# Kernel optimization log

Hardware: AMD Instinct MI355X
Metric: run time of the kernel (lower is better)

The kernel has to match this reference:

```python
import jax, jax.numpy as jnp
import numpy as np

B, N, H, A = 2048, 49, 1024, 512


def setup_inputs() -> dict:
    key = jax.random.key(0)
    ks = jax.random.split(key, 9)
    s_h = 1.0 / np.sqrt(H)
    s_a = 1.0 / np.sqrt(A)
    return {
        "hidden": jax.random.normal(ks[0], (B, H), jnp.float32),
        "img_features": jax.random.normal(ks[1], (B, N, H), jnp.float32),
        "coverage": jax.random.uniform(ks[2], (B, N), jnp.float32),
        "W_h": jax.random.uniform(ks[3], (H, A), jnp.float32, -s_h, s_h),
        "b_h": jax.random.uniform(ks[4], (A,), jnp.float32, -s_h, s_h),
        "W_img": jax.random.uniform(ks[5], (H, A), jnp.float32, -s_h, s_h),
        "b_img": jax.random.uniform(ks[6], (A,), jnp.float32, -s_h, s_h),
        "W_cov": jax.random.uniform(ks[7], (1, A), jnp.float32, -1.0, 1.0),
        "v": jax.random.uniform(ks[8], (A,), jnp.float32, -s_a, s_a),
    }


def reference(hidden, img_features, coverage, W_h, b_h, W_img, b_img, W_cov, v):
    # h_proj: (B, 1, A); img_proj: (B, N, A)
    h_proj = (hidden @ W_h + b_h)[:, None, :]
    img_proj = jnp.einsum("bnh,ha->bna", img_features, W_img) + b_img
    # coverage projection: (B, N, 1) @ (1, A) -> (B, N, A)
    cov_proj = coverage[:, :, None] * W_cov[0]
    energy = jnp.tanh(h_proj + img_proj + cov_proj)
    scores = jnp.einsum("bna,a->bn", energy, v)  # (B, N)
    alpha = jax.nn.softmax(scores, axis=1)
    context = jnp.einsum("bn,bnh->bh", alpha, img_features)
    return (context, alpha)
```

## Files before the change

### kernel.cpp

```cpp
#include <hip/hip_runtime.h>
#include <cstdint>
#include <cstddef>

#define B_ 2048
#define N_ 49
#define H_ 1024
#define A_ 512
#define M_ (B_*N_)

typedef __attribute__((ext_vector_type(8))) short short8;
typedef __attribute__((ext_vector_type(8))) unsigned short ushort8;
typedef __attribute__((ext_vector_type(4))) float f32x4;
typedef unsigned int u32;

__device__ inline unsigned short f2bf(float f){
  union { float f; unsigned u; } v; v.f = f;
  unsigned r = v.u + 0x7FFFu + ((v.u >> 16) & 1u);
  return (unsigned short)(r >> 16);
}
__device__ inline float bf2f(unsigned short h){
  union { u32 u; float f; } v; v.u = ((u32)h) << 16; return v.f;
}
__device__ inline float fast_tanh(float x){
  float e = __expf(2.0f*x);
  return 1.0f - 2.0f/(e + 1.0f);
}
__device__ inline void gl16(const void* g, void* l){
  __builtin_amdgcn_global_load_lds((const __attribute__((address_space(1))) u32*)g,
                                   (__attribute__((address_space(3))) u32*)l, 16, 0, 0);
}

__global__ __launch_bounds__(256) void k_transpose(
    const float* __restrict__ Wh, const float* __restrict__ Wimg,
    unsigned short* __restrict__ WtH, unsigned short* __restrict__ WtImg){
  const float* src = blockIdx.y ? Wimg : Wh;
  unsigned short* dst = blockIdx.y ? WtImg : WtH;
  int tk = (blockIdx.x & 31) * 32;
  int ta = (blockIdx.x >> 5) * 32;
  __shared__ unsigned short tile[32][33];
  int t = threadIdx.x;
  int r = t >> 3, c4 = t & 7;
  float4 vv = *(const float4*)(src + (size_t)(tk + r)*A_ + ta + c4*4);
  tile[c4*4+0][r] = f2bf(vv.x);
  tile[c4*4+1][r] = f2bf(vv.y);
  tile[c4*4+2][r] = f2bf(vv.z);
  tile[c4*4+3][r] = f2bf(vv.w);
  __syncthreads();
  ushort4 o;
  o.x = tile[r][c4*4+0]; o.y = tile[r][c4*4+1];
  o.z = tile[r][c4*4+2]; o.w = tile[r][c4*4+3];
  *(ushort4*)(dst + (size_t)(ta + r)*H_ + tk + c4*4) = o;
}

__global__ __launch_bounds__(256) void k_convert(
    const float* __restrict__ src, unsigned short* __restrict__ dst, size_t n8){
  size_t i = (size_t)blockIdx.x*256 + threadIdx.x;
  size_t stride = (size_t)gridDim.x*256;
  const float4* s4 = (const float4*)src;
  ushort8* d8 = (ushort8*)dst;
  for (; i < n8; i += stride){
    float4 a = s4[2*i], b = s4[2*i+1];
    ushort8 o;
    o[0]=f2bf(a.x); o[1]=f2bf(a.y); o[2]=f2bf(a.z); o[3]=f2bf(a.w);
    o[4]=f2bf(b.x); o[5]=f2bf(b.y); o[6]=f2bf(b.z); o[7]=f2bf(b.w);
    d8[i] = o;
  }
}

#define BK 64
#define LDK 72

__device__ inline void gemm_tile(const float* __restrict__ Asrc,
                                 const unsigned short* __restrict__ Wt,
                                 int m0, int a0, f32x4 acc[4][4],
                                 unsigned short (*sA)[LDK], unsigned short (*sB)[LDK]){
  const int t = threadIdx.x;
  const int l = t & 63, w = t >> 6;
  const int wr = w >> 1, wc = w & 1;
  const int g = l >> 4, c = l & 15;
  #pragma unroll
  for (int m=0;m<4;m++)
    #pragma unroll
    for (int n=0;n<4;n++)
      acc[m][n] = f32x4{0.f,0.f,0.f,0.f};

  for (int k0 = 0; k0 < H_; k0 += BK){
    #pragma unroll
    for (int i=0;i<8;i++){
      int f = i*256 + t;
      int row = f >> 4, c4 = f & 15;
      float4 vv = *(const float4*)(Asrc + (size_t)(m0+row)*H_ + k0 + c4*4);
      ushort4 h; h.x=f2bf(vv.x); h.y=f2bf(vv.y); h.z=f2bf(vv.z); h.w=f2bf(vv.w);
      *(ushort4*)&sA[row][c4*4] = h;
    }
    #pragma unroll
    for (int i=0;i<8;i++){
      int f = i*256 + t;
      int row = f >> 4, c4 = f & 15;
      *(ushort4*)&sB[row][c4*4] = *(const ushort4*)(Wt + (size_t)(a0+row)*H_ + k0 + c4*4);
    }
    __syncthreads();
    #pragma unroll
    for (int kk=0; kk<BK; kk+=32){
      short8 aF[4], bF[4];
      #pragma unroll
      for (int m=0;m<4;m++) aF[m] = *(const short8*)&sA[wr*64 + m*16 + c][kk + g*8];
      #pragma unroll
      for (int n=0;n<4;n++) bF[n] = *(const short8*)&sB[wc*64 + n*16 + c][kk + g*8];
      #pragma unroll
      for (int m=0;m<4;m++)
        #pragma unroll
        for (int n=0;n<4;n++)
          acc[m][n] = __builtin_amdgcn_mfma_f32_16x16x32_bf16(aF[m], bF[n], acc[m][n], 0, 0, 0);
    }
    __syncthreads();
  }
}

__global__ __launch_bounds__(256) void k_hproj(
    const float* __restrict__ hidden, const unsigned short* __restrict__ WtH,
    const float* __restrict__ b_h, float* __restrict__ hproj){
  __shared__ __align__(16) unsigned short sA[128][LDK];
  __shared__ __align__(16) unsigned short sB[128][LDK];
  f32x4 acc[4][4];
  int m0 = blockIdx.x * 128, a0 = blockIdx.y * 128;
  gemm_tile(hidden, WtH, m0, a0, acc, sA, sB);
  const int l = threadIdx.x & 63, w = threadIdx.x >> 6;
  const int wr = w >> 1, wc = w & 1, g = l >> 4, c = l & 15;
  #pragma unroll
  for (int n=0;n<4;n++){
    int col = a0 + wc*64 + n*16 + c;
    float bh = b_h[col];
    #pragma unroll
    for (int m=0;m<4;m++)
      #pragma unroll
      for (int r=0;r<4;r++){
        int rowg = m0 + wr*64 + m*16 + g*4 + r;
        hproj[(size_t)rowg*A_ + col] = acc[m][n][r] + bh;
      }
  }
}

__global__ __launch_bounds__(512, 2) void k_scores_p8(
    const unsigned short* __restrict__ Ab, const unsigned short* __restrict__ Wt,
    const float* __restrict__ hproj, const float* __restrict__ b_img,
    const float* __restrict__ cov, const float* __restrict__ Wcov,
    const float* __restrict__ v, float* __restrict__ scoresP){
  __shared__ __align__(16) char lds[131072];
  const int t = threadIdx.x;
  const int l = t & 63, w = t >> 6;
  const int wr = w >> 2, wc = w & 3;
  const int g = l >> 4, c = l & 15;
  const int cm = (c & 7) << 4;

  const int nwg = (M_/256)*(A_/256);
  int bid = blockIdx.x;
  int wg = (bid & 7)*(nwg/8) + (bid >> 3);
  const int m0 = (wg >> 1) * 256;
  const int a0 = (wg & 1) * 256;

  const int rsub = l >> 3;
  const int ksw  = ((l & 7) ^ rsub) * 8;

  f32x4 acc[8][4] = {};

  auto unit = [&](int d, int opoff, int h, int row0,
                  const unsigned short* src, int prow, int k0){
    gl16(src + (size_t)(prow + h*128 + row0 + w*8 + rsub)*H_ + k0 + ksw,
         lds + d*65536 + opoff + h*16384 + row0*128 + w*1024);
  };

  const int abase_s = wr*16384;
  const int bbase_s = 32768 + (wc>>1)*16384;
  const int brow    = (wc & 1)*64;

  auto phase_mfma = [&](int cur, int mh, int kb){
    short8 aF[4], bF[4];
    #pragma unroll
    for (int i=0;i<4;i++)
      aF[i] = *(const short8*)(lds + cur + abase_s + (mh*64 + i*16 + c)*128 + ((kb*64 + g*16) ^ cm));
    #pragma unroll
    for (int n=0;n<4;n++)
      bF[n] = *(const short8*)(lds + cur + bbase_s + (brow + n*16 + c)*128 + ((kb*64 + g*16) ^ cm));
    asm volatile("s_waitcnt lgkmcnt(0)" ::: "memory");
    __builtin_amdgcn_sched_barrier(0);
    __builtin_amdgcn_s_setprio(1);
    #pragma unroll
    for (int i=0;i<4;i++)
      #pragma unroll
      for (int n=0;n<4;n++)
        acc[mh*4+i][n] = __builtin_amdgcn_mfma_f32_16x16x32_bf16(aF[i], bF[n], acc[mh*4+i][n], 0, 0, 0);
    __builtin_amdgcn_s_setprio(0);
  };

  unit(0, 32768, 0, 0,  Wt, a0, 0);
  unit(0, 32768, 0, 64, Wt, a0, 0);
  unit(0, 32768, 1, 0,  Wt, a0, 0);
  unit(0, 32768, 1, 64, Wt, a0, 0);
  unit(0, 0,     0, 0,  Ab, m0, 0);
  unit(0, 0,     1, 0,  Ab, m0, 0);
  unit(0, 0,     0, 64, Ab, m0, 0);
  unit(0, 0,     1, 64, Ab, m0, 0);

  for (int tt=0; tt<16; ++tt){
    const int cur = (tt & 1) << 16;
    const int nd  = (tt + 1) & 1;
    const int nk  = (tt + 1) * 64;
    const bool pf = (tt < 15);

    if (pf){ unit(nd, 32768, 0, 0, Wt, a0, nk); unit(nd, 32768, 0, 64, Wt, a0, nk);
             asm volatile("s_waitcnt vmcnt(4)" ::: "memory"); }
    else   { asm volatile("s_waitcnt vmcnt(2)" ::: "memory"); }
    asm volatile("s_barrier" ::: "memory");
    phase_mfma(cur, 0, 0);
    asm volatile("s_barrier" ::: "memory");

    if (pf){ unit(nd, 32768, 1, 0, Wt, a0, nk); unit(nd, 32768, 1, 64, Wt, a0, nk); }
    asm volatile("s_barrier" ::: "memory");
    phase_mfma(cur, 0, 1);
    asm volatile("s_barrier" ::: "memory");

    if (pf){ unit(nd, 0, 0, 0, Ab, m0, nk); unit(nd, 0, 1, 0, Ab, m0, nk);
             asm volatile("s_waitcnt vmcnt(6)" ::: "memory"); }
    else   { asm volatile("s_waitcnt vmcnt(0)" ::: "memory"); }
    asm volatile("s_barrier" ::: "memory");
    phase_mfma(cur, 1, 0);
    asm volatile("s_barrier" ::: "memory");

    if (pf){ unit(nd, 0, 0, 64, Ab, m0, nk); unit(nd, 0, 1, 64, Ab, m0, nk); }
    asm volatile("s_barrier" ::: "memory");
    phase_mfma(cur, 1, 1);
    asm volatile("s_barrier" ::: "memory");
  }

  float* sS = (float*)lds;
  float* sH = (float*)lds + 256;
  const int bFirst = m0 / N_;
  const int nB = (m0 + 255)/N_ - bFirst + 1;
  if (t < 256) sS[t] = 0.f;
  for (int idx = t; idx < nB*256; idx += 512){
    int bb = idx >> 8, a = idx & 255;
    sH[bb*256 + a] = hproj[(size_t)(bFirst + bb)*A_ + a0 + a];
  }
  __syncthreads();

  float vv[4], bi[4], wcv[4];
  #pragma unroll
  for (int n=0;n<4;n++){
    int colg = a0 + wc*64 + n*16 + c;
    vv[n] = v[colg]; bi[n] = b_img[colg]; wcv[n] = Wcov[colg];
  }
  #pragma unroll
  for (int m=0;m<8;m++){
    #pragma unroll
    for (int r=0;r<4;r++){
      int rowl = wr*128 + m*16 + g*4 + r;
      int bb = (m0 + rowl) / N_ - bFirst;
      float cv = cov[m0 + rowl];
      float s = 0.f;
      #pragma unroll
      for (int n=0;n<4;n++){
        float x = acc[m][n][r] + sH[bb*256 + wc*64 + n*16 + c] + bi[n] + cv*wcv[n];
        s += fast_tanh(x) * vv[n];
      }
      s += __shfl_xor(s, 1, 16);
      s += __shfl_xor(s, 2, 16);
      s += __shfl_xor(s, 4, 16);
      s += __shfl_xor(s, 8, 16);
      if (c == 0) atomicAdd(&sS[rowl], s);
    }
  }
  __syncthreads();
  if (t < 256) scoresP[(size_t)(a0 >> 8)*M_ + m0 + t] = sS[t];
}

__global__ __launch_bounds__(256) void k_ctx_b(
    const unsigned short* __restrict__ imgb, const float* __restrict__ scoresP,
    float* __restrict__ outCtx, float* __restrict__ outAlpha){
  int b = blockIdx.x;
  __shared__ float sAl[N_];
  int t = threadIdx.x;
  if (t < 64){
    float s = -1e30f;
    if (t < N_){
      size_t rg = (size_t)b*N_ + t;
      s = scoresP[rg] + scoresP[(size_t)M_ + rg];
    }
    float m = s;
    #pragma unroll
    for (int off=32; off>=1; off>>=1) m = fmaxf(m, __shfl_xor(m, off));
    float e = (t < N_) ? __expf(s - m) : 0.f;
    float sum = e;
    #pragma unroll
    for (int off=32; off>=1; off>>=1) sum += __shfl_xor(sum, off);
    float al = e / sum;
    if (t < N_){ sAl[t] = al; outAlpha[(size_t)b*N_ + t] = al; }
  }
  __syncthreads();
  float4 acc = {0.f,0.f,0.f,0.f};
  #pragma unroll 7
  for (int n=0;n<N_;n++){
    float al = sAl[n];
    ushort4 x = *(const ushort4*)(imgb + ((size_t)b*N_ + n)*H_ + t*4);
    acc.x += al*bf2f(x.x); acc.y += al*bf2f(x.y);
    acc.z += al*bf2f(x.z); acc.w += al*bf2f(x.w);
  }
  *(float4*)(outCtx + (size_t)b*H_ + t*4) = acc;
}

__global__ __launch_bounds__(256) void k_scores_f(
    const float* __restrict__ img, const unsigned short* __restrict__ WtImg,
    const float* __restrict__ hproj, const float* __restrict__ b_img,
    const float* __restrict__ cov, const float* __restrict__ Wcov,
    const float* __restrict__ v, float* __restrict__ scores){
  __shared__ __align__(16) unsigned short sA[128][LDK];
  __shared__ __align__(16) unsigned short sB[128][LDK];
  __shared__ float sH[4][128];
  f32x4 acc[4][4];
  int m0 = blockIdx.x * 128, a0 = blockIdx.y * 128;
  gemm_tile(img, WtImg, m0, a0, acc, sA, sB);
  int bFirst = m0 / N_;
  int bLast  = (m0 + 127) / N_;
  int nB = bLast - bFirst + 1;
  for (int idx = threadIdx.x; idx < nB*128; idx += 256){
    int bb = idx >> 7, a = idx & 127;
    sH[bb][a] = hproj[(size_t)(bFirst + bb)*A_ + a0 + a];
  }
  __syncthreads();
  const int l = threadIdx.x & 63, w = threadIdx.x >> 6;
  const int wr = w >> 1, wc = w & 1, g = l >> 4, c = l & 15;
  float vv[4], bi[4], wcv[4];
  #pragma unroll
  for (int n=0;n<4;n++){
    int col = a0 + wc*64 + n*16 + c;
    vv[n] = v[col]; bi[n] = b_img[col]; wcv[n] = Wcov[col];
  }
  #pragma unroll
  for (int m=0;m<4;m++)
    #pragma unroll
    for (int r=0;r<4;r++){
      int rowg = m0 + wr*64 + m*16 + g*4 + r;
      int bb = rowg / N_;
      float cv = cov[rowg];
      float s = 0.f;
      #pragma unroll
      for (int n=0;n<4;n++){
        float x = acc[m][n][r] + sH[bb - bFirst][wc*64 + n*16 + c] + bi[n] + cv*wcv[n];
        s += fast_tanh(x) * vv[n];
      }
      s += __shfl_xor(s, 1, 16);
      s += __shfl_xor(s, 2, 16);
      s += __shfl_xor(s, 4, 16);
      s += __shfl_xor(s, 8, 16);
      if (c == 0) atomicAdd(&scores[rowg], s);
    }
}

__global__ __launch_bounds__(256) void k_ctx_f(
    const float* __restrict__ img, const float* __restrict__ scores,
    float* __restrict__ outCtx, float* __restrict__ outAlpha){
  int b = blockIdx.x;
  __shared__ float sAl[N_];
  int t = threadIdx.x;
  if (t < 64){
    float s = (t < N_) ? scores[(size_t)b*N_ + t] : -1e30f;
    float m = s;
    #pragma unroll
    for (int off=32; off>=1; off>>=1) m = fmaxf(m, __shfl_xor(m, off));
    float e = (t < N_) ? __expf(s - m) : 0.f;
    float sum = e;
    #pragma unroll
    for (int off=32; off>=1; off>>=1) sum += __shfl_xor(sum, off);
    float al = e / sum;
    if (t < N_){ sAl[t] = al; outAlpha[(size_t)b*N_ + t] = al; }
  }
  __syncthreads();
  const float4* ib = (const float4*)(img + (size_t)b*N_*H_);
  float4 acc = {0.f,0.f,0.f,0.f};
  for (int n=0;n<N_;n++){
    float al = sAl[n];
    float4 x = ib[n*(H_/4) + t];
    acc.x += al*x.x; acc.y += al*x.y; acc.z += al*x.z; acc.w += al*x.w;
  }
  *(float4*)(outCtx + (size_t)b*H_ + t*4) = acc;
}

extern "C" void kernel_launch(void* const* d_in, const int* in_sizes, int n_in,
                              void* d_out, int out_size, void* d_ws, size_t ws_size,
                              hipStream_t stream){
  const float* hidden = (const float*)d_in[0];
  const float* img    = (const float*)d_in[1];
  const float* cov    = (const float*)d_in[2];
  const float* W_h    = (const float*)d_in[3];
  const float* b_h    = (const float*)d_in[4];
  const float* W_img  = (const float*)d_in[5];
  const float* b_img  = (const float*)d_in[6];
  const float* W_cov  = (const float*)d_in[7];
  const float* v      = (const float*)d_in[8];

  char* ws = (char*)d_ws;
  unsigned short* WtH   = (unsigned short*)ws;
  unsigned short* WtImg = (unsigned short*)(ws + (1u<<20));
  float* hproj   = (float*)(ws + (2u<<20));
  float* scoresP = (float*)(ws + (6u<<20));
  unsigned short* imgb = (unsigned short*)(ws + (8u<<20));

  float* outCtx   = (float*)d_out;
  float* outAlpha = outCtx + (size_t)B_*H_;

  const size_t needed = (8ull<<20) + (size_t)M_*H_*2;

  k_transpose<<<dim3(512, 2), 256, 0, stream>>>(W_h, W_img, WtH, WtImg);
  k_hproj<<<dim3(B_/128, A_/128), 256, 0, stream>>>(hidden, WtH, b_h, hproj);

  if (ws_size >= needed){
    k_convert<<<2048, 256, 0, stream>>>(img, imgb, (size_t)M_*H_/8);
    k_scores_p8<<<(M_/256)*(A_/256), 512, 0, stream>>>(imgb, WtImg, hproj, b_img, cov, W_cov, v, scoresP);
    k_ctx_b<<<B_, 256, 0, stream>>>(imgb, scoresP, outCtx, outAlpha);
  } else {
    hipMemsetAsync(scoresP, 0, (size_t)M_*sizeof(float), stream);
    k_scores_f<<<dim3(M_/128, A_/128), 256, 0, stream>>>(img, WtImg, hproj, b_img, cov, W_cov, v, scoresP);
    k_ctx_f<<<B_, 256, 0, stream>>>(img, scoresP, outCtx, outAlpha);
  }
}
```

Baseline: 347.2 us.

## Fuse score GEMM, softmax and context into one per-batch-group kernel

Replaces the split scores kernel and the separate context kernel with a single kernel. Each block owns 5 whole batches (245 rows padded to 256) and loops over both A halves itself, reducing scores in LDS. It then does the softmax and the alpha-weighted context sum in the same block. This removes the partial-scores round trip through global memory and a second launch, and the context pass can reread image rows that were just loaded and are likely still cached. The next half's tile loads are issued before the first epilogue so they overlap it. In exchange about 4% of GEMM rows are padding, and the grid shrinks to 410 large blocks, which may balance poorly across CUs.

```diff
diff --git a/kernel.cpp b/kernel.cpp
--- a/kernel.cpp
+++ b/kernel.cpp
@@ -7,6 +7,8 @@
 #define H_ 1024
 #define A_ 512
 #define M_ (B_*N_)
+#define NBB 5
+#define NBLK ((B_ + NBB - 1)/NBB)
 
 typedef __attribute__((ext_vector_type(8))) short short8;
 typedef __attribute__((ext_vector_type(8))) unsigned short ushort8;
@@ -141,33 +143,45 @@
   }
 }
 
-__global__ __launch_bounds__(512, 2) void k_scores_p8(
-    const unsigned short* __restrict__ Ab, const unsigned short* __restrict__ Wt,
+__global__ __launch_bounds__(512, 2) void k_fused2(
+    const unsigned short* __restrict__ imgb, const unsigned short* __restrict__ Wt,
     const float* __restrict__ hproj, const float* __restrict__ b_img,
     const float* __restrict__ cov, const float* __restrict__ Wcov,
-    const float* __restrict__ v, float* __restrict__ scoresP){
+    const float* __restrict__ v,
+    float* __restrict__ outCtx, float* __restrict__ outAlpha){
   __shared__ __align__(16) char lds[131072];
+  __shared__ float sSx[256];
+  __shared__ float sHx[NBB][256];
+  __shared__ float sAl[256];
+
   const int t = threadIdx.x;
   const int l = t & 63, w = t >> 6;
   const int wr = w >> 2, wc = w & 3;
   const int g = l >> 4, c = l & 15;
   const int cm = (c & 7) << 4;
 
-  const int nwg = (M_/256)*(A_/256);
-  int bid = blockIdx.x;
-  int wg = (bid & 7)*(nwg/8) + (bid >> 3);
-  const int m0 = (wg >> 1) * 256;
-  const int a0 = (wg & 1) * 256;
+  const int bm = blockIdx.x;
+  const int bb0 = bm * NBB;
+  const int NB = min(NBB, B_ - bb0);
+  const int mrows = NB * N_;
+  const int m0 = bb0 * N_;
+
+  if (t < 256) sSx[t] = 0.f;
 
   const int rsub = l >> 3;
   const int ksw  = ((l & 7) ^ rsub) * 8;
 
-  f32x4 acc[8][4] = {};
-
-  auto unit = [&](int d, int opoff, int h, int row0,
-                  const unsigned short* src, int prow, int k0){
-    gl16(src + (size_t)(prow + h*128 + row0 + w*8 + rsub)*H_ + k0 + ksw,
-         lds + d*65536 + opoff + h*16384 + row0*128 + w*1024);
+  f32x4 acc[8][4];
+
+  auto unitB = [&](int d, int a0, int h, int row0, int k0){
+    gl16(Wt + (size_t)(a0 + h*128 + row0 + w*8 + rsub)*H_ + k0 + ksw,
+         lds + d*65536 + 32768 + h*16384 + row0*128 + w*1024);
+  };
+  auto unitA = [&](int d, int h, int row0, int k0){
+    int prow = m0 + h*128 + row0 + w*8 + rsub;
+    if (prow >= M_) prow = 0;
+    gl16(imgb + (size_t)prow*H_ + k0 + ksw,
+         lds + d*65536 + h*16384 + row0*128 + w*1024);
   };
 
   const int abase_s = wr*16384;
@@ -193,119 +207,131 @@
     __builtin_amdgcn_s_setprio(0);
   };
 
-  unit(0, 32768, 0, 0,  Wt, a0, 0);
-  unit(0, 32768, 0, 64, Wt, a0, 0);
-  unit(0, 32768, 1, 0,  Wt, a0, 0);
-  unit(0, 32768, 1, 64, Wt, a0, 0);
-  unit(0, 0,     0, 0,  Ab, m0, 0);
-  unit(0, 0,     1, 0,  Ab, m0, 0);
-  unit(0, 0,     0, 64, Ab, m0, 0);
-  unit(0, 0,     1, 64, Ab, m0, 0);
-
-  for (int tt=0; tt<16; ++tt){
-    const int cur = (tt & 1) << 16;
-    const int nd  = (tt + 1) & 1;
-    const int nk  = (tt + 1) * 64;
-    const bool pf = (tt < 15);
-
-    if (pf){ unit(nd, 32768, 0, 0, Wt, a0, nk); unit(nd, 32768, 0, 64, Wt, a0, nk);
-             asm volatile("s_waitcnt vmcnt(4)" ::: "memory"); }
-    else   { asm volatile("s_waitcnt vmcnt(2)" ::: "memory"); }
-    asm volatile("s_barrier" ::: "memory");
-    phase_mfma(cur, 0, 0);
-    asm volatile("s_barrier" ::: "memory");
-
-    if (pf){ unit(nd, 32768, 1, 0, Wt, a0, nk); unit(nd, 32768, 1, 64, Wt, a0, nk); }
-    asm volatile("s_barrier" ::: "memory");
-    phase_mfma(cur, 0, 1);
-    asm volatile("s_barrier" ::: "memory");
-
-    if (pf){ unit(nd, 0, 0, 0, Ab, m0, nk); unit(nd, 0, 1, 0, Ab, m0, nk);
-             asm volatile("s_waitcnt vmcnt(6)" ::: "memory"); }
-    else   { asm volatile("s_waitcnt vmcnt(0)" ::: "memory"); }
-    asm volatile("s_barrier" ::: "memory");
-    phase_mfma(cur, 1, 0);
-    asm volatile("s_barrier" ::: "memory");
-
-    if (pf){ unit(nd, 0, 0, 64, Ab, m0, nk); unit(nd, 0, 1, 64, Ab, m0, nk); }
-    asm volatile("s_barrier" ::: "memory");
-    phase_mfma(cur, 1, 1);
-    asm volatile("s_barrier" ::: "memory");
-  }
-
-  float* sS = (float*)lds;
-  float* sH = (float*)lds + 256;
-  const int bFirst = m0 / N_;
-  const int nB = (m0 + 255)/N_ - bFirst + 1;
-  if (t < 256) sS[t] = 0.f;
-  for (int idx = t; idx < nB*256; idx += 512){
-    int bb = idx >> 8, a = idx & 255;
-    sH[bb*256 + a] = hproj[(size_t)(bFirst + bb)*A_ + a0 + a];
-  }
-  __syncthreads();
-
-  float vv[4], bi[4], wcv[4];
-  #pragma unroll
-  for (int n=0;n<4;n++){
-    int colg = a0 + wc*64 + n*16 + c;
-    vv[n] = v[colg]; bi[n] = b_img[colg]; wcv[n] = Wcov[colg];
-  }
-  #pragma unroll
-  for (int m=0;m<8;m++){
-    #pragma unroll
-    for (int r=0;r<4;r++){
-      int rowl = wr*128 + m*16 + g*4 + r;
-      int bb = (m0 + rowl) / N_ - bFirst;
-      float cv = cov[m0 + rowl];
-      float s = 0.f;
-      #pragma unroll
-      for (int n=0;n<4;n++){
-        float x = acc[m][n][r] + sH[bb*256 + wc*64 + n*16 + c] + bi[n] + cv*wcv[n];
-        s += fast_tanh(x) * vv[n];
+  auto prologue = [&](int a0){
+    unitB(0, a0, 0, 0, 0);  unitB(0, a0, 0, 64, 0);
+    unitB(0, a0, 1, 0, 0);  unitB(0, a0, 1, 64, 0);
+    unitA(0, 0, 0, 0);      unitA(0, 1, 0, 0);
+    unitA(0, 0, 64, 0);     unitA(0, 1, 64, 0);
+  };
+
+  auto kloop = [&](int a0){
+    for (int tt=0; tt<16; ++tt){
+      const int cur = (tt & 1) << 16;
+      const int nd  = (tt + 1) & 1;
+      const int nk  = (tt + 1) * 64;
+      const bool pf = (tt < 15);
+
+      if (pf){ unitB(nd, a0, 0, 0, nk); unitB(nd, a0, 0, 64, nk);
+               asm volatile("s_waitcnt vmcnt(4)" ::: "memory"); }
+      else   { asm volatile("s_waitcnt vmcnt(2)" ::: "memory"); }
+      asm volatile("s_barrier" ::: "memory");
+      phase_mfma(cur, 0, 0);
+      asm volatile("s_barrier" ::: "memory");
+
+      if (pf){ unitB(nd, a0, 1, 0, nk); unitB(nd, a0, 1, 64, nk); }
+      asm volatile("s_barrier" ::: "memory");
+      phase_mfma(cur, 0, 1);
+      asm volatile("s_barrier" ::: "memory");
+
+      if (pf){ unitA(nd, 0, 0, nk); unitA(nd, 1, 0, nk);
+               asm volatile("s_waitcnt vmcnt(6)" ::: "memory"); }
+      else   { asm volatile("s_waitcnt vmcnt(0)" ::: "memory"); }
+      asm volatile("s_barrier" ::: "memory");
+      phase_mfma(cur, 1, 0);
+      asm volatile("s_barrier" ::: "memory");
+
+      if (pf){ unitA(nd, 0, 64, nk); unitA(nd, 1, 64, nk); }
+      asm volatile("s_barrier" ::: "memory");
+      phase_mfma(cur, 1, 1);
+      asm volatile("s_barrier" ::: "memory");
+    }
+  };
+
+  auto epi = [&](int a0){
+    for (int idx = t; idx < NB*256; idx += 512){
+      int bb = idx >> 8, a = idx & 255;
+      sHx[bb][a] = hproj[(size_t)(bb0 + bb)*A_ + a0 + a];
+    }
+    __syncthreads();
+    float vv[4], bi[4], wcv[4];
+    #pragma unroll
+    for (int n=0;n<4;n++){
+      int colg = a0 + wc*64 + n*16 + c;
+      vv[n] = v[colg]; bi[n] = b_img[colg]; wcv[n] = Wcov[colg];
+    }
+    #pragma unroll
+    for (int m=0;m<8;m++){
+      #pragma unroll
+      for (int r=0;r<4;r++){
+        int rowl = wr*128 + m*16 + g*4 + r;
+        if (rowl < mrows){
+          int bb = rowl / N_;
+          float cv = cov[m0 + rowl];
+          float s = 0.f;
+          #pragma unroll
+          for (int n=0;n<4;n++){
+            float x = acc[m][n][r] + sHx[bb][wc*64 + n*16 + c] + bi[n] + cv*wcv[n];
+            s += fast_tanh(x) * vv[n];
+          }
+          s += __shfl_xor(s, 1, 16);
+          s += __shfl_xor(s, 2, 16);
+          s += __shfl_xor(s, 4, 16);
+          s += __shfl_xor(s, 8, 16);
+          if (c == 0) atomicAdd(&sSx[rowl], s);
+        }
       }
-      s += __shfl_xor(s, 1, 16);
-      s += __shfl_xor(s, 2, 16);
-      s += __shfl_xor(s, 4, 16);
-      s += __shfl_xor(s, 8, 16);
-      if (c == 0) atomicAdd(&sS[rowl], s);
-    }
-  }
-  __syncthreads();
-  if (t < 256) scoresP[(size_t)(a0 >> 8)*M_ + m0 + t] = sS[t];
-}
-
-__global__ __launch_bounds__(256) void k_ctx_b(
-    const unsigned short* __restrict__ imgb, const float* __restrict__ scoresP,
-    float* __restrict__ outCtx, float* __restrict__ outAlpha){
-  int b = blockIdx.x;
-  __shared__ float sAl[N_];
-  int t = threadIdx.x;
-  if (t < 64){
-    float s = -1e30f;
-    if (t < N_){
-      size_t rg = (size_t)b*N_ + t;
-      s = scoresP[rg] + scoresP[(size_t)M_ + rg];
-    }
-    float m = s;
-    #pragma unroll
-    for (int off=32; off>=1; off>>=1) m = fmaxf(m, __shfl_xor(m, off));
-    float e = (t < N_) ? __expf(s - m) : 0.f;
+    }
+    __syncthreads();
+  };
+
+  #pragma unroll
+  for (int m=0;m<8;m++)
+    #pragma unroll
+    for (int n=0;n<4;n++) acc[m][n] = f32x4{0.f,0.f,0.f,0.f};
+  prologue(0);
+  kloop(0);
+  prologue(256);
+  epi(0);
+
+  #pragma unroll
+  for (int m=0;m<8;m++)
+    #pragma unroll
+    for (int n=0;n<4;n++) acc[m][n] = f32x4{0.f,0.f,0.f,0.f};
+  kloop(256);
+  epi(256);
+
+  if (w < NB){
+    int b = w;
+    float s = (l < N_) ? sSx[b*N_ + l] : -1e30f;
+    float mx = s;
+    #pragma unroll
+    for (int off=32; off>=1; off>>=1) mx = fmaxf(mx, __shfl_xor(mx, off));
+    float e = (l < N_) ? __expf(s - mx) : 0.f;
     float sum = e;
     #pragma unroll
     for (int off=32; off>=1; off>>=1) sum += __shfl_xor(sum, off);
     float al = e / sum;
-    if (t < N_){ sAl[t] = al; outAlpha[(size_t)b*N_ + t] = al; }
+    if (l < N_){
+      sAl[b*N_ + l] = al;
+      outAlpha[(size_t)(m0 + b*N_ + l)] = al;
+    }
   }
   __syncthreads();
-  float4 acc = {0.f,0.f,0.f,0.f};
-  #pragma unroll 7
-  for (int n=0;n<N_;n++){
-    float al = sAl[n];
-    ushort4 x = *(const ushort4*)(imgb + ((size_t)b*N_ + n)*H_ + t*4);
-    acc.x += al*bf2f(x.x); acc.y += al*bf2f(x.y);
-    acc.z += al*bf2f(x.z); acc.w += al*bf2f(x.w);
-  }
-  *(float4*)(outCtx + (size_t)b*H_ + t*4) = acc;
+
+  const int th = t >> 8;
+  const int tc = t & 255;
+  for (int b = th; b < NB; b += 2){
+    float ax=0.f, ay=0.f, az=0.f, aw=0.f;
+    #pragma unroll 7
+    for (int n=0; n<N_; ++n){
+      float al = sAl[b*N_ + n];
+      ushort4 u = *(const ushort4*)(imgb + (size_t)(m0 + b*N_ + n)*H_ + tc*4);
+      ax += al*bf2f(u.x); ay += al*bf2f(u.y);
+      az += al*bf2f(u.z); aw += al*bf2f(u.w);
+    }
+    float4 o; o.x=ax; o.y=ay; o.z=az; o.w=aw;
+    *(float4*)(outCtx + (size_t)(bb0 + b)*H_ + tc*4) = o;
+  }
 }
 
 __global__ __launch_bounds__(256) void k_scores_f(
@@ -402,7 +428,7 @@
   unsigned short* WtH   = (unsigned short*)ws;
   unsigned short* WtImg = (unsigned short*)(ws + (1u<<20));
   float* hproj   = (float*)(ws + (2u<<20));
-  float* scoresP = (float*)(ws + (6u<<20));
+  float* scoresF = (float*)(ws + (6u<<20));
   unsigned short* imgb = (unsigned short*)(ws + (8u<<20));
 
   float* outCtx   = (float*)d_out;
@@ -415,11 +441,11 @@
 
   if (ws_size >= needed){
     k_convert<<<2048, 256, 0, stream>>>(img, imgb, (size_t)M_*H_/8);
-    k_scores_p8<<<(M_/256)*(A_/256), 512, 0, stream>>>(imgb, WtImg, hproj, b_img, cov, W_cov, v, scoresP);
-    k_ctx_b<<<B_, 256, 0, stream>>>(imgb, scoresP, outCtx, outAlpha);
+    k_fused2<<<NBLK, 512, 0, stream>>>(imgb, WtImg, hproj, b_img, cov, W_cov, v,
+                                       outCtx, outAlpha);
   } else {
-    hipMemsetAsync(scoresP, 0, (size_t)M_*sizeof(float), stream);
-    k_scores_f<<<dim3(M_/128, A_/128), 256, 0, stream>>>(img, WtImg, hproj, b_img, cov, W_cov, v, scoresP);
-    k_ctx_f<<<B_, 256, 0, stream>>>(img, scoresP, outCtx, outAlpha);
-  }
-}
+    hipMemsetAsync(scoresF, 0, (size_t)M_*sizeof(float), stream);
+    k_scores_f<<<dim3(M_/128, A_/128), 256, 0, stream>>>(img, WtImg, hproj, b_img, cov, W_cov, v, scoresF);
+    k_ctx_f<<<B_, 256, 0, stream>>>(img, scoresF, outCtx, outAlpha);
+  }
+}
```

New measurement: 450.7 us. 1.3x slower.

## Halve scores GEMM K-tile to 32 to cut LDS and raise occupancy

Applied to the files above, without the earlier changes.

The fused scores GEMM now stages 32-wide K slices instead of 64, so the double-buffered LDS footprint drops from 128 KB to 64 KB. Launch bounds ask for 4 blocks per CU instead of 2. The swizzle, load mapping and pipeline are reworked into 32 iterations with two phases each. This trades more barriers and loop overhead per unit of work for higher occupancy and latency hiding. The register budget at 4x512 threads may force spills with an 8x4 accumulator array.

```diff
diff --git a/kernel.cpp b/kernel.cpp
--- a/kernel.cpp
+++ b/kernel.cpp
@@ -141,17 +141,17 @@
   }
 }
 
-__global__ __launch_bounds__(512, 2) void k_scores_p8(
+__global__ __launch_bounds__(512, 4) void k_scores_q(
     const unsigned short* __restrict__ Ab, const unsigned short* __restrict__ Wt,
     const float* __restrict__ hproj, const float* __restrict__ b_img,
     const float* __restrict__ cov, const float* __restrict__ Wcov,
     const float* __restrict__ v, float* __restrict__ scoresP){
-  __shared__ __align__(16) char lds[131072];
+  __shared__ __align__(16) char lds[65536];
   const int t = threadIdx.x;
   const int l = t & 63, w = t >> 6;
   const int wr = w >> 2, wc = w & 3;
   const int g = l >> 4, c = l & 15;
-  const int cm = (c & 7) << 4;
+  const int cm = (c & 3) << 4;
 
   const int nwg = (M_/256)*(A_/256);
   int bid = blockIdx.x;
@@ -159,29 +159,24 @@
   const int m0 = (wg >> 1) * 256;
   const int a0 = (wg & 1) * 256;
 
-  const int rsub = l >> 3;
-  const int ksw  = ((l & 7) ^ rsub) * 8;
+  const int rsub = l >> 2;
+  const int ksw  = ((l & 3) ^ (rsub & 3)) * 8;
 
   f32x4 acc[8][4] = {};
 
-  auto unit = [&](int d, int opoff, int h, int row0,
-                  const unsigned short* src, int prow, int k0){
-    gl16(src + (size_t)(prow + h*128 + row0 + w*8 + rsub)*H_ + k0 + ksw,
-         lds + d*65536 + opoff + h*16384 + row0*128 + w*1024);
+  auto unit = [&](int d, int isB, int row0, const unsigned short* src, int prow, int k0){
+    gl16(src + (size_t)(prow + row0 + w*16 + rsub)*H_ + k0 + ksw,
+         lds + isB*32768 + d*16384 + (row0 + w*16)*64);
   };
 
-  const int abase_s = wr*16384;
-  const int bbase_s = 32768 + (wc>>1)*16384;
-  const int brow    = (wc & 1)*64;
-
-  auto phase_mfma = [&](int cur, int mh, int kb){
+  auto phase_mfma = [&](int d, int mh){
     short8 aF[4], bF[4];
     #pragma unroll
     for (int i=0;i<4;i++)
-      aF[i] = *(const short8*)(lds + cur + abase_s + (mh*64 + i*16 + c)*128 + ((kb*64 + g*16) ^ cm));
+      aF[i] = *(const short8*)(lds + d*16384 + (wr*128 + mh*64 + i*16 + c)*64 + ((g*16) ^ cm));
     #pragma unroll
     for (int n=0;n<4;n++)
-      bF[n] = *(const short8*)(lds + cur + bbase_s + (brow + n*16 + c)*128 + ((kb*64 + g*16) ^ cm));
+      bF[n] = *(const short8*)(lds + 32768 + d*16384 + (wc*64 + n*16 + c)*64 + ((g*16) ^ cm));
     asm volatile("s_waitcnt lgkmcnt(0)" ::: "memory");
     __builtin_amdgcn_sched_barrier(0);
     __builtin_amdgcn_s_setprio(1);
@@ -193,43 +188,27 @@
     __builtin_amdgcn_s_setprio(0);
   };
 
-  unit(0, 32768, 0, 0,  Wt, a0, 0);
-  unit(0, 32768, 0, 64, Wt, a0, 0);
-  unit(0, 32768, 1, 0,  Wt, a0, 0);
-  unit(0, 32768, 1, 64, Wt, a0, 0);
-  unit(0, 0,     0, 0,  Ab, m0, 0);
-  unit(0, 0,     1, 0,  Ab, m0, 0);
-  unit(0, 0,     0, 64, Ab, m0, 0);
-  unit(0, 0,     1, 64, Ab, m0, 0);
-
-  for (int tt=0; tt<16; ++tt){
-    const int cur = (tt & 1) << 16;
+  unit(0, 1, 0,   Wt, a0, 0);
+  unit(0, 1, 128, Wt, a0, 0);
+  unit(0, 0, 0,   Ab, m0, 0);
+  unit(0, 0, 128, Ab, m0, 0);
+
+  for (int tt=0; tt<32; ++tt){
+    const int cur = tt & 1;
     const int nd  = (tt + 1) & 1;
-    const int nk  = (tt + 1) * 64;
-    const bool pf = (tt < 15);
-
-    if (pf){ unit(nd, 32768, 0, 0, Wt, a0, nk); unit(nd, 32768, 0, 64, Wt, a0, nk);
-             asm volatile("s_waitcnt vmcnt(4)" ::: "memory"); }
-    else   { asm volatile("s_waitcnt vmcnt(2)" ::: "memory"); }
-    asm volatile("s_barrier" ::: "memory");
-    phase_mfma(cur, 0, 0);
-    asm volatile("s_barrier" ::: "memory");
-
-    if (pf){ unit(nd, 32768, 1, 0, Wt, a0, nk); unit(nd, 32768, 1, 64, Wt, a0, nk); }
-    asm volatile("s_barrier" ::: "memory");
-    phase_mfma(cur, 0, 1);
-    asm volatile("s_barrier" ::: "memory");
-
-    if (pf){ unit(nd, 0, 0, 0, Ab, m0, nk); unit(nd, 0, 1, 0, Ab, m0, nk);
-             asm volatile("s_waitcnt vmcnt(6)" ::: "memory"); }
+    const int nk  = (tt + 1) * 32;
+    const bool pf = (tt < 31);
+
+    if (pf){ unit(nd, 1, 0, Wt, a0, nk); unit(nd, 1, 128, Wt, a0, nk);
+             asm volatile("s_waitcnt vmcnt(2)" ::: "memory"); }
     else   { asm volatile("s_waitcnt vmcnt(0)" ::: "memory"); }
     asm volatile("s_barrier" ::: "memory");
-    phase_mfma(cur, 1, 0);
+    phase_mfma(cur, 0);
     asm volatile("s_barrier" ::: "memory");
 
-    if (pf){ unit(nd, 0, 0, 64, Ab, m0, nk); unit(nd, 0, 1, 64, Ab, m0, nk); }
+    if (pf){ unit(nd, 0, 0, Ab, m0, nk); unit(nd, 0, 128, Ab, m0, nk); }
     asm volatile("s_barrier" ::: "memory");
-    phase_mfma(cur, 1, 1);
+    phase_mfma(cur, 1);
     asm volatile("s_barrier" ::: "memory");
   }
 
@@ -415,7 +394,7 @@
 
   if (ws_size >= needed){
     k_convert<<<2048, 256, 0, stream>>>(img, imgb, (size_t)M_*H_/8);
-    k_scores_p8<<<(M_/256)*(A_/256), 512, 0, stream>>>(imgb, WtImg, hproj, b_img, cov, W_cov, v, scoresP);
+    k_scores_q<<<(M_/256)*(A_/256), 512, 0, stream>>>(imgb, WtImg, hproj, b_img, cov, W_cov, v, scoresP);
     k_ctx_b<<<B_, 256, 0, stream>>>(imgb, scoresP, outCtx, outAlpha);
   } else {
     hipMemsetAsync(scoresP, 0, (size_t)M_*sizeof(float), stream);
```

Result: slower. 1.091 ms (+214.2%).
